# Kernel optimization log

Measured on AMD Instinct MI355X. Metric: run time of the kernel, lower is better.

## Reference

```python
import jax, jax.numpy as jnp
import numpy as np

N = 64      # num_neighbors + 1
H = 512     # hidden_size
T = 1024    # history length


def setup_inputs() -> dict:
    key = jax.random.key(0)
    ks = jax.random.split(key, 10)
    s = 1.0 / np.sqrt(H)  # PyTorch LSTM/Linear init scale
    return {
        "in_recent_values": jax.random.normal(ks[0], (N,), dtype=jnp.float32),
        "in_reputation_history": jax.random.normal(ks[1], (N, T), dtype=jnp.float32),
        # per-module LSTM params (input_size=1), gate order i,f,g,o
        "W_ih": jax.random.uniform(ks[2], (N, 4 * H), jnp.float32, -s, s),      # [N,4H] (input_size=1 squeezed)
        "W_hh": jax.random.uniform(ks[3], (N, 4 * H, H), jnp.float32, -s, s),   # [N,4H,H]
        "b_ih": jax.random.uniform(ks[4], (N, 4 * H), jnp.float32, -s, s),
        "b_hh": jax.random.uniform(ks[5], (N, 4 * H), jnp.float32, -s, s),
        # per-module output Linear(H+1 -> 1)
        "lin_W": jax.random.uniform(ks[6], (N, H + 1), jnp.float32, -s, s),
        "lin_b": jax.random.uniform(ks[7], (N,), jnp.float32, -s, s),
        # final Linear(N -> 1)
        "final_W": jax.random.uniform(ks[8], (N,), jnp.float32, -1.0 / np.sqrt(N), 1.0 / np.sqrt(N)),
        "final_b": jax.random.uniform(ks[9], (1,), jnp.float32, -1.0 / np.sqrt(N), 1.0 / np.sqrt(N)),
    }


def _batched_lstm_last_h(history, W_ih, W_hh, b_ih, b_hh):
    # history: [N,T]. Precompute input contribution for all steps: [T,N,4H]
    x_proj = history[:, :, None] * W_ih[:, None, :] + (b_ih + b_hh)[:, None, :]
    x_proj = jnp.swapaxes(x_proj, 0, 1)  # [T,N,4H]

    def step(carry, x_t):
        h, c = carry  # [N,H] each
        gates = x_t + jnp.einsum("nh,ngh->ng", h, W_hh)  # [N,4H]
        i, f, g, o = jnp.split(gates, 4, axis=-1)
        i = jax.nn.sigmoid(i)
        f = jax.nn.sigmoid(f)
        g = jnp.tanh(g)
        o = jax.nn.sigmoid(o)
        c = f * c + i * g
        h = o * jnp.tanh(c)
        return (h, c), None

    h0 = jnp.zeros((N, H), dtype=history.dtype)
    (h_last, _), _ = jax.lax.scan(step, (h0, h0), x_proj)
    return h_last  # [N,H]


def reference(in_recent_values, in_reputation_history, W_ih, W_hh, b_ih, b_hh,
              lin_W, lin_b, final_W, final_b):
    h_last = _batched_lstm_last_h(in_reputation_history, W_ih, W_hh, b_ih, b_hh)
    # per-module linear on [h_last, current_reading] -> scalar each
    feat = jnp.concatenate([h_last, in_recent_values[:, None]], axis=1)  # [N,H+1]
    per_mod = jnp.sum(feat * lin_W, axis=1) + lin_b                      # [N]
    out = per_mod @ final_W + final_b                                    # [1]
    return out
```

## Files before the change

### kernel.cpp

```cpp
#include <hip/hip_runtime.h>
#include <hip/hip_fp16.h>
#include <cstddef>

#define NMOD 64
#define HID 512
#define TSTEPS 1024
#define G4 2048

#define WOFF_PERMOD 0
#define WOFF_HX     16384
#define WOFF_W16    524288
#define W16_BYTES   ((size_t)NMOD * G4 * HID * 2)
#define WS_NEED     (WOFF_W16 + W16_BYTES)

__device__ __forceinline__ float fsig(float x)  { return 1.0f / (1.0f + __expf(-x)); }
__device__ __forceinline__ float ftanh_(float x){ return 1.0f - 2.0f / (__expf(2.0f * x) + 1.0f); }

__device__ __forceinline__ float adot2(unsigned a, unsigned b, float c) {
    float d;
    asm("v_dot2_f32_f16 %0, %1, %2, %3" : "=v"(d) : "v"(a), "v"(b), "v"(c));
    return d;
}
__device__ __forceinline__ float dot4(uint4 wv, uint4 hv, float acc) {
    acc = adot2(wv.x, hv.x, acc);
    acc = adot2(wv.y, hv.y, acc);
    acc = adot2(wv.z, hv.z, acc);
    acc = adot2(wv.w, hv.w, acc);
    return acc;
}

template<int CTRL>
__device__ __forceinline__ float dppf(float x) {
    int xi = __builtin_bit_cast(int, x);
    int r = __builtin_amdgcn_update_dpp(0, xi, CTRL, 0xF, 0xF, true);
    return __builtin_bit_cast(float, r);
}

__global__ __launch_bounds__(256) void conv_kernel(const float* __restrict__ src,
                                                   __half* __restrict__ dst) {
    const size_t i = ((size_t)blockIdx.x * 256 + threadIdx.x) * 8;
    const float4 a = *reinterpret_cast<const float4*>(src + i);
    const float4 b = *reinterpret_cast<const float4*>(src + i + 4);
    __half2 h0 = __floats2half2_rn(a.x, a.y);
    __half2 h1 = __floats2half2_rn(a.z, a.w);
    __half2 h2 = __floats2half2_rn(b.x, b.y);
    __half2 h3 = __floats2half2_rn(b.z, b.w);
    uint4 o;
    o.x = *reinterpret_cast<unsigned*>(&h0);
    o.y = *reinterpret_cast<unsigned*>(&h1);
    o.z = *reinterpret_cast<unsigned*>(&h2);
    o.w = *reinterpret_cast<unsigned*>(&h3);
    *reinterpret_cast<uint4*>(dst + i) = o;
}

__global__
__attribute__((amdgpu_flat_work_group_size(512, 512), amdgpu_waves_per_eu(2, 2)))
void lstm_res_kernel(
    const float* __restrict__ recent,
    const float* __restrict__ history,
    const float* __restrict__ W_ih,
    const float* __restrict__ b_ih,
    const float* __restrict__ b_hh,
    const float* __restrict__ lin_W,
    const float* __restrict__ lin_b,
    const unsigned* __restrict__ w16u,
    unsigned long long* hx,
    float* __restrict__ per_mod)
{
    const int bid = blockIdx.x;
    const int m = (bid & 7) * 8 + (bid >> 5);
    const int b = (bid >> 3) & 3;
    const int tid = threadIdx.x;
    const int rg = tid >> 4;
    const int cg = tid & 15;

    __shared__ unsigned w_lds[32768];
    __shared__ unsigned h_pk[256];
    __shared__ float gates_sh[512];
    __shared__ float hist_sh[TSTEPS];
    __shared__ float red_sh[8];

    for (int i = tid; i < TSTEPS; i += 512)
        hist_sh[i] = history[(size_t)m * TSTEPS + i];

    const size_t rowbase = (size_t)m * G4 * 256;
    uint4 w[12][4];
    #pragma unroll
    for (int r = 0; r < 12; ++r) {
        const int l = rg * 16 + r;
        const int gr = ((l >> 7) << 9) + (b << 7) + (l & 127);
        #pragma unroll
        for (int kk = 0; kk < 4; ++kk) {
            const int c = (((b + kk) & 3) << 4) + cg;
            w[r][kk] = *(const uint4*)(w16u + rowbase + (size_t)gr * 256 + c * 4);
        }
    }
    #pragma unroll
    for (int r2 = 0; r2 < 4; ++r2) {
        const int l = rg * 16 + 12 + r2;
        const int gr = ((l >> 7) << 9) + (b << 7) + (l & 127);
        #pragma unroll
        for (int kk = 0; kk < 4; ++kk) {
            const int c  = (((b + kk) & 3) << 4) + cg;
            const int wc = (((kk + rg) & 3) << 4) + cg;
            *(uint4*)&w_lds[((rg * 4 + r2) * 64 + wc) * 4] =
                *(const uint4*)(w16u + rowbase + (size_t)gr * 256 + c * 4);
        }
    }

    const int rev = ((cg & 1) << 3) | ((cg & 2) << 1) | ((cg & 4) >> 1) | ((cg & 8) >> 3);
    const int l_own = rg * 16 + rev;
    const int gr_own = ((l_own >> 7) << 9) + (b << 7) + (l_own & 127);
    const float wib_own  = W_ih[(size_t)m * G4 + gr_own];
    const float bias_own = b_ih[(size_t)m * G4 + gr_own] + b_hh[(size_t)m * G4 + gr_own];

    const bool is_writer = (tid < 128);
    const bool is_reader = (tid >= 128 && tid < 320);
    const int  rr    = tid - 128;
    const int  widx  = (((b + 1 + (rr >> 6)) & 3) << 6) + (rr & 63);

    float c0 = 0.0f;

    if (tid < 256) h_pk[tid] = 0u;

    gates_sh[l_own] = hist_sh[0] * wib_own + bias_own;

    for (int t = 0; t < TSTEPS - 1; ++t) {
        __syncthreads();
        const unsigned seq = (unsigned)(t + 1);
        const size_t pbase = (size_t)(seq & 1) * (NMOD * 256) + (size_t)m * 256;

        unsigned long long pv = 0;
        if (is_writer) {
            const float gi = fsig(gates_sh[tid]);
            const float gf = fsig(gates_sh[128 + tid]);
            const float gg = ftanh_(gates_sh[256 + tid]);
            const float go = fsig(gates_sh[384 + tid]);
            c0 = gf * c0 + gi * gg;
            const float hv = go * ftanh_(c0);
            const float ho = __shfl_xor(hv, 1, 64);
            if ((tid & 1) == 0) {
                __half2 hh = __floats2half2_rn(hv, ho);
                const unsigned pay = *reinterpret_cast<unsigned*>(&hh);
                const int word = tid >> 1;
                __hip_atomic_store(&hx[pbase + b * 64 + word],
                                   ((unsigned long long)seq << 32) | pay,
                                   __ATOMIC_RELAXED, __HIP_MEMORY_SCOPE_AGENT);
                h_pk[b * 64 + word] = pay;
            }
        } else if (is_reader) {
            pv = __hip_atomic_load(&hx[pbase + widx],
                                   __ATOMIC_RELAXED, __HIP_MEMORY_SCOPE_AGENT);
        }
        __syncthreads();

        float acc[16];
        #pragma unroll
        for (int r = 0; r < 16; ++r) acc[r] = 0.0f;
        {
            const uint4 hq = *(const uint4*)&h_pk[(b << 6) + cg * 4];
            #pragma unroll
            for (int r = 0; r < 12; ++r) acc[r] = dot4(w[r][0], hq, acc[r]);
            const int wc0 = ((rg & 3) << 4) + cg;
            #pragma unroll
            for (int r2 = 0; r2 < 4; ++r2) {
                const uint4 lw = *(const uint4*)&w_lds[((rg * 4 + r2) * 64 + wc0) * 4];
                acc[12 + r2] = dot4(lw, hq, acc[12 + r2]);
            }
        }

        if (is_reader) {
            while ((unsigned)(pv >> 32) != seq)
                pv = __hip_atomic_load(&hx[pbase + widx],
                                       __ATOMIC_RELAXED, __HIP_MEMORY_SCOPE_AGENT);
            h_pk[widx] = (unsigned)pv;
        }
        __syncthreads();

        #pragma unroll
        for (int kk = 1; kk < 4; ++kk) {
            const uint4 hq = *(const uint4*)&h_pk[((((b + kk) & 3)) << 6) + cg * 4];
            #pragma unroll
            for (int r = 0; r < 12; ++r) acc[r] = dot4(w[r][kk], hq, acc[r]);
            const int wc = (((kk + rg) & 3) << 4) + cg;
            #pragma unroll
            for (int r2 = 0; r2 < 4; ++r2) {
                const uint4 lw = *(const uint4*)&w_lds[((rg * 4 + r2) * 64 + wc) * 4];
                acc[12 + r2] = dot4(lw, hq, acc[12 + r2]);
            }
        }

        #pragma unroll
        for (int k = 0; k < 8; ++k) {
            const float send = (cg & 1) ? acc[k] : acc[8 + k];
            const float recv = dppf<0xB1>(send);
            acc[k] = ((cg & 1) ? acc[8 + k] : acc[k]) + recv;
        }
        #pragma unroll
        for (int k = 0; k < 4; ++k) {
            const float send = (cg & 2) ? acc[k] : acc[4 + k];
            const float recv = dppf<0x4E>(send);
            acc[k] = ((cg & 2) ? acc[4 + k] : acc[k]) + recv;
        }
        #pragma unroll
        for (int k = 0; k < 2; ++k) {
            const float send = (cg & 4) ? acc[k] : acc[2 + k];
            const float recv = __shfl_xor(send, 4, 64);
            acc[k] = ((cg & 4) ? acc[2 + k] : acc[k]) + recv;
        }
        {
            const float send = (cg & 8) ? acc[0] : acc[1];
            const float recv = __shfl_xor(send, 8, 64);
            acc[0] = ((cg & 8) ? acc[1] : acc[0]) + recv;
        }

        gates_sh[l_own] = acc[0] + hist_sh[t + 1] * wib_own + bias_own;
    }

    __syncthreads();
    {
        const unsigned seq = (unsigned)TSTEPS;
        const size_t pbase = (size_t)(seq & 1) * (NMOD * 256) + (size_t)m * 256;
        if (is_writer) {
            const float gi = fsig(gates_sh[tid]);
            const float gf = fsig(gates_sh[128 + tid]);
            const float gg = ftanh_(gates_sh[256 + tid]);
            const float go = fsig(gates_sh[384 + tid]);
            c0 = gf * c0 + gi * gg;
            const float hv = go * ftanh_(c0);
            const float ho = __shfl_xor(hv, 1, 64);
            if ((tid & 1) == 0) {
                __half2 hh = __floats2half2_rn(hv, ho);
                const unsigned pay = *reinterpret_cast<unsigned*>(&hh);
                const int word = tid >> 1;
                __hip_atomic_store(&hx[pbase + b * 64 + word],
                                   ((unsigned long long)seq << 32) | pay,
                                   __ATOMIC_RELAXED, __HIP_MEMORY_SCOPE_AGENT);
                h_pk[b * 64 + word] = pay;
            }
        }
        if (b == 0) {
            if (is_reader) {
                unsigned long long pv;
                do {
                    pv = __hip_atomic_load(&hx[pbase + widx],
                                           __ATOMIC_RELAXED, __HIP_MEMORY_SCOPE_AGENT);
                } while ((unsigned)(pv >> 32) != seq);
                h_pk[widx] = (unsigned)pv;
            }
            __syncthreads();
            float v = 0.0f;
            if (tid < 256) {
                const __half2 u = *reinterpret_cast<const __half2*>(&h_pk[tid]);
                const float* lwp = lin_W + (size_t)m * (HID + 1);
                v = __half2float(u.x) * lwp[2 * tid] + __half2float(u.y) * lwp[2 * tid + 1];
            }
            #pragma unroll
            for (int s2 = 32; s2; s2 >>= 1) v += __shfl_xor(v, s2, 64);
            if ((tid & 63) == 0) red_sh[tid >> 6] = v;
            __syncthreads();
            if (tid == 0) {
                float s = 0.0f;
                #pragma unroll
                for (int wv2 = 0; wv2 < 8; ++wv2) s += red_sh[wv2];
                s += recent[m] * lin_W[(size_t)m * (HID + 1) + HID] + lin_b[m];
                per_mod[m] = s;
            }
        }
    }
}

__global__ __launch_bounds__(1024) void lstm_module_kernel(
    const float* __restrict__ recent,
    const float* __restrict__ history,
    const float* __restrict__ W_ih,
    const float* __restrict__ W_hh,
    const float* __restrict__ b_ih,
    const float* __restrict__ b_hh,
    const float* __restrict__ lin_W,
    const float* __restrict__ lin_b,
    float* __restrict__ per_mod)
{
    const int n = blockIdx.x;
    const int tid = threadIdx.x;

    __shared__ float h_sh[HID];
    __shared__ float gates_sh[G4];
    __shared__ float wib_sh[G4];
    __shared__ float bias_sh[G4];
    __shared__ float hist_sh[TSTEPS];

    for (int i = tid; i < G4; i += 1024) {
        wib_sh[i]  = W_ih[(size_t)n * G4 + i];
        bias_sh[i] = b_ih[(size_t)n * G4 + i] + b_hh[(size_t)n * G4 + i];
    }
    for (int i = tid; i < TSTEPS; i += 1024) hist_sh[i] = history[(size_t)n * TSTEPS + i];
    if (tid < HID) h_sh[tid] = 0.0f;
    float c_reg = 0.0f;
    __syncthreads();

    const int sub = tid & 15;
    const int rid = tid >> 4;
    const float* Wbase = W_hh + (size_t)n * G4 * HID;

    for (int t = 0; t < TSTEPS; ++t) {
        const float x = hist_sh[t];
        float hreg[32];
        #pragma unroll
        for (int j = 0; j < 8; ++j) {
            const float4 hv = *reinterpret_cast<const float4*>(&h_sh[sub * 4 + j * 64]);
            hreg[4 * j + 0] = hv.x; hreg[4 * j + 1] = hv.y;
            hreg[4 * j + 2] = hv.z; hreg[4 * j + 3] = hv.w;
        }
        for (int p = 0; p < 32; ++p) {
            const int r = p * 64 + rid;
            const float* wr = Wbase + (size_t)r * HID + sub * 4;
            float acc = 0.0f;
            #pragma unroll
            for (int j = 0; j < 8; ++j) {
                const float4 wv = *reinterpret_cast<const float4*>(wr + j * 64);
                acc += wv.x * hreg[4*j+0] + wv.y * hreg[4*j+1]
                     + wv.z * hreg[4*j+2] + wv.w * hreg[4*j+3];
            }
            acc += __shfl_xor(acc, 1, 64);
            acc += __shfl_xor(acc, 2, 64);
            acc += __shfl_xor(acc, 4, 64);
            acc += __shfl_xor(acc, 8, 64);
            if (sub == 0) gates_sh[r] = acc + x * wib_sh[r] + bias_sh[r];
        }
        __syncthreads();
        if (tid < HID) {
            const float ig = fsig(gates_sh[tid]);
            const float fg = fsig(gates_sh[HID + tid]);
            const float gg = ftanh_(gates_sh[2 * HID + tid]);
            const float og = fsig(gates_sh[3 * HID + tid]);
            c_reg = fg * c_reg + ig * gg;
            h_sh[tid] = og * ftanh_(c_reg);
        }
        __syncthreads();
    }

    if (tid < HID) {
        float v = h_sh[tid] * lin_W[(size_t)n * (HID + 1) + tid];
        #pragma unroll
        for (int m2 = 32; m2; m2 >>= 1) v += __shfl_xor(v, m2, 64);
        if ((tid & 63) == 0) gates_sh[tid >> 6] = v;
    }
    __syncthreads();
    if (tid == 0) {
        float s = 0.0f;
        #pragma unroll
        for (int w = 0; w < HID / 64; ++w) s += gates_sh[w];
        s += recent[n] * lin_W[(size_t)n * (HID + 1) + HID] + lin_b[n];
        per_mod[n] = s;
    }
}

__global__ void finish_kernel(const float* __restrict__ per_mod,
                              const float* __restrict__ final_W,
                              const float* __restrict__ final_b,
                              float* __restrict__ out)
{
    const int l = threadIdx.x;
    float v = per_mod[l] * final_W[l];
    #pragma unroll
    for (int m = 32; m; m >>= 1) v += __shfl_xor(v, m, 64);
    if (l == 0) out[0] = v + final_b[0];
}

extern "C" void kernel_launch(void* const* d_in, const int* in_sizes, int n_in,
                              void* d_out, int out_size, void* d_ws, size_t ws_size,
                              hipStream_t stream) {
    const float* recent  = (const float*)d_in[0];
    const float* history = (const float*)d_in[1];
    const float* W_ih    = (const float*)d_in[2];
    const float* W_hh    = (const float*)d_in[3];
    const float* b_ih    = (const float*)d_in[4];
    const float* b_hh    = (const float*)d_in[5];
    const float* lin_W   = (const float*)d_in[6];
    const float* lin_b   = (const float*)d_in[7];
    const float* final_W = (const float*)d_in[8];
    const float* final_b = (const float*)d_in[9];
    float* out = (float*)d_out;
    float* per_mod = (float*)d_ws;

    if (ws_size >= WS_NEED) {
        __half* w16 = (__half*)((char*)d_ws + WOFF_W16);
        unsigned long long* hx = (unsigned long long*)((char*)d_ws + WOFF_HX);

        hipMemsetAsync(d_ws, 0, WOFF_W16, stream);

        const int conv_blocks = (int)((size_t)NMOD * G4 * HID / 8 / 256);
        conv_kernel<<<conv_blocks, 256, 0, stream>>>(W_hh, w16);

        lstm_res_kernel<<<NMOD * 4, 512, 0, stream>>>(
            recent, history, W_ih, b_ih, b_hh, lin_W, lin_b,
            (const unsigned*)w16, hx, per_mod);
    } else {
        lstm_module_kernel<<<NMOD, 1024, 0, stream>>>(
            recent, history, W_ih, W_hh, b_ih, b_hh, lin_W, lin_b, per_mod);
    }
    finish_kernel<<<1, 64, 0, stream>>>(per_mod, final_W, final_b, out);
}
```

Baseline: 2.444 ms.

## Replace dot2 GEMV with MFMA 16x16x32 f16 on fragment-prepacked weights

The recurrent matvec per step moves from v_dot2 instructions plus a DPP/shuffle cross-lane reduction to MFMA 16x16x32 f16 instructions. The h vector is broadcast as the B operand. The conversion kernel now writes W_hh directly in MFMA fragment order, so each wave loads its register and LDS tiles with contiguous reads. This removes the per-step butterfly reduction, but it wastes most of the MFMA columns (only one useful column) and adds MFMA latency to the serial recurrence.

Result: slower. 2.509 ms (+2.6%).

```diff
diff --git a/kernel.cpp b/kernel.cpp
--- a/kernel.cpp
+++ b/kernel.cpp
@@ -13,49 +13,52 @@
 #define W16_BYTES   ((size_t)NMOD * G4 * HID * 2)
 #define WS_NEED     (WOFF_W16 + W16_BYTES)
 
+typedef _Float16 half8_t __attribute__((ext_vector_type(8)));
+typedef float    f32x4_t __attribute__((ext_vector_type(4)));
+
 __device__ __forceinline__ float fsig(float x)  { return 1.0f / (1.0f + __expf(-x)); }
 __device__ __forceinline__ float ftanh_(float x){ return 1.0f - 2.0f / (__expf(2.0f * x) + 1.0f); }
 
-__device__ __forceinline__ float adot2(unsigned a, unsigned b, float c) {
-    float d;
-    asm("v_dot2_f32_f16 %0, %1, %2, %3" : "=v"(d) : "v"(a), "v"(b), "v"(c));
-    return d;
-}
-__device__ __forceinline__ float dot4(uint4 wv, uint4 hv, float acc) {
-    acc = adot2(wv.x, hv.x, acc);
-    acc = adot2(wv.y, hv.y, acc);
-    acc = adot2(wv.z, hv.z, acc);
-    acc = adot2(wv.w, hv.w, acc);
-    return acc;
-}
-
-template<int CTRL>
-__device__ __forceinline__ float dppf(float x) {
-    int xi = __builtin_bit_cast(int, x);
-    int r = __builtin_amdgcn_update_dpp(0, xi, CTRL, 0xF, 0xF, true);
-    return __builtin_bit_cast(float, r);
-}
-
-__global__ __launch_bounds__(256) void conv_kernel(const float* __restrict__ src,
-                                                   __half* __restrict__ dst) {
-    const size_t i = ((size_t)blockIdx.x * 256 + threadIdx.x) * 8;
-    const float4 a = *reinterpret_cast<const float4*>(src + i);
-    const float4 b = *reinterpret_cast<const float4*>(src + i + 4);
+__device__ __forceinline__ half8_t h8(uint4 u) { return __builtin_bit_cast(half8_t, u); }
+
+#define MFMA_F16(a, b, c) __builtin_amdgcn_mfma_f32_16x16x32_f16((a), (b), (c), 0, 0, 0)
+
+__global__ __launch_bounds__(256) void conv_frag_kernel(const float* __restrict__ src,
+                                                        unsigned* __restrict__ dst) {
+    const unsigned t_lin = blockIdx.x * 256 + threadIdx.x;
+    const unsigned chunk = t_lin >> 6, u = t_lin & 63;
+    const unsigned l = ((u & 3) << 4) | (u >> 2);
+    const unsigned t = (chunk << 6) | l;
+
+    const int ll = t & 63;
+    const int j  = (t >> 6) & 15;
+    const int mt = (t >> 10) & 3;
+    const int w  = (t >> 12) & 7;
+    const int b  = (t >> 15) & 3;
+    const int m  = (int)(t >> 17);
+    const int kc = (4 * b + j) & 15;
+    const int g  = ll >> 4, r16 = ll & 15;
+    const int lr = w * 64 + mt * 16 + r16;
+    const int gr = (lr >> 7) * 512 + b * 128 + (lr & 127);
+
+    const float* sp = src + ((size_t)m * G4 + gr) * HID + kc * 32 + g * 8;
+    const float4 a = *reinterpret_cast<const float4*>(sp);
+    const float4 c = *reinterpret_cast<const float4*>(sp + 4);
     __half2 h0 = __floats2half2_rn(a.x, a.y);
     __half2 h1 = __floats2half2_rn(a.z, a.w);
-    __half2 h2 = __floats2half2_rn(b.x, b.y);
-    __half2 h3 = __floats2half2_rn(b.z, b.w);
+    __half2 h2 = __floats2half2_rn(c.x, c.y);
+    __half2 h3 = __floats2half2_rn(c.z, c.w);
     uint4 o;
     o.x = *reinterpret_cast<unsigned*>(&h0);
     o.y = *reinterpret_cast<unsigned*>(&h1);
     o.z = *reinterpret_cast<unsigned*>(&h2);
     o.w = *reinterpret_cast<unsigned*>(&h3);
-    *reinterpret_cast<uint4*>(dst + i) = o;
+    *reinterpret_cast<uint4*>(dst + (size_t)t * 4) = o;
 }
 
 __global__
 __attribute__((amdgpu_flat_work_group_size(512, 512), amdgpu_waves_per_eu(2, 2)))
-void lstm_res_kernel(
+void lstm_mfma_kernel(
     const float* __restrict__ recent,
     const float* __restrict__ history,
     const float* __restrict__ W_ih,
@@ -63,7 +66,7 @@
     const float* __restrict__ b_hh,
     const float* __restrict__ lin_W,
     const float* __restrict__ lin_b,
-    const unsigned* __restrict__ w16u,
+    const unsigned* __restrict__ wf,
     unsigned long long* hx,
     float* __restrict__ per_mod)
 {
@@ -71,10 +74,12 @@
     const int m = (bid & 7) * 8 + (bid >> 5);
     const int b = (bid >> 3) & 3;
     const int tid = threadIdx.x;
-    const int rg = tid >> 4;
-    const int cg = tid & 15;
-
-    __shared__ unsigned w_lds[32768];
+    const int w   = tid >> 6;
+    const int l   = tid & 63;
+    const int g   = l >> 4;
+    const int c16 = l & 15;
+
+    __shared__ uint4 w_lds[8][4][4][64];
     __shared__ unsigned h_pk[256];
     __shared__ float gates_sh[512];
     __shared__ float hist_sh[TSTEPS];
@@ -83,47 +88,48 @@
     for (int i = tid; i < TSTEPS; i += 512)
         hist_sh[i] = history[(size_t)m * TSTEPS + i];
 
-    const size_t rowbase = (size_t)m * G4 * 256;
-    uint4 w[12][4];
+    const uint4* fb = (const uint4*)wf + (size_t)((m * 4 + b) * 8 + w) * 4096;
+    uint4 wr[4][12];
     #pragma unroll
-    for (int r = 0; r < 12; ++r) {
-        const int l = rg * 16 + r;
-        const int gr = ((l >> 7) << 9) + (b << 7) + (l & 127);
-        #pragma unroll
-        for (int kk = 0; kk < 4; ++kk) {
-            const int c = (((b + kk) & 3) << 4) + cg;
-            w[r][kk] = *(const uint4*)(w16u + rowbase + (size_t)gr * 256 + c * 4);
-        }
-    }
+    for (int mt = 0; mt < 4; ++mt)
+        #pragma unroll
+        for (int j = 0; j < 12; ++j)
+            wr[mt][j] = fb[(mt * 16 + j) * 64 + l];
     #pragma unroll
-    for (int r2 = 0; r2 < 4; ++r2) {
-        const int l = rg * 16 + 12 + r2;
-        const int gr = ((l >> 7) << 9) + (b << 7) + (l & 127);
-        #pragma unroll
-        for (int kk = 0; kk < 4; ++kk) {
-            const int c  = (((b + kk) & 3) << 4) + cg;
-            const int wc = (((kk + rg) & 3) << 4) + cg;
-            *(uint4*)&w_lds[((rg * 4 + r2) * 64 + wc) * 4] =
-                *(const uint4*)(w16u + rowbase + (size_t)gr * 256 + c * 4);
-        }
-    }
-
-    const int rev = ((cg & 1) << 3) | ((cg & 2) << 1) | ((cg & 4) >> 1) | ((cg & 8) >> 3);
-    const int l_own = rg * 16 + rev;
-    const int gr_own = ((l_own >> 7) << 9) + (b << 7) + (l_own & 127);
-    const float wib_own  = W_ih[(size_t)m * G4 + gr_own];
-    const float bias_own = b_ih[(size_t)m * G4 + gr_own] + b_hh[(size_t)m * G4 + gr_own];
+    for (int mt = 0; mt < 4; ++mt)
+        #pragma unroll
+        for (int j2 = 0; j2 < 4; ++j2)
+            w_lds[w][mt][j2][l] = fb[(mt * 16 + 12 + j2) * 64 + l];
+
+    float wib4[4], bias4[4];
+    if (c16 < 4) {
+        #pragma unroll
+        for (int e = 0; e < 4; ++e) {
+            const int lr = w * 64 + c16 * 16 + g * 4 + e;
+            const int gr = (lr >> 7) * 512 + b * 128 + (lr & 127);
+            wib4[e]  = W_ih[(size_t)m * G4 + gr];
+            bias4[e] = b_ih[(size_t)m * G4 + gr] + b_hh[(size_t)m * G4 + gr];
+        }
+    }
 
     const bool is_writer = (tid < 128);
     const bool is_reader = (tid >= 128 && tid < 320);
-    const int  rr    = tid - 128;
-    const int  widx  = (((b + 1 + (rr >> 6)) & 3) << 6) + (rr & 63);
+    const int  rr   = tid - 128;
+    const int  widx = (((b + 1 + (rr >> 6)) & 3) << 6) + (rr & 63);
 
     float c0 = 0.0f;
-
     if (tid < 256) h_pk[tid] = 0u;
-
-    gates_sh[l_own] = hist_sh[0] * wib_own + bias_own;
+    __syncthreads();
+
+    if (c16 < 4) {
+        const float x0 = hist_sh[0];
+        float4 o;
+        o.x = x0 * wib4[0] + bias4[0];
+        o.y = x0 * wib4[1] + bias4[1];
+        o.z = x0 * wib4[2] + bias4[2];
+        o.w = x0 * wib4[3] + bias4[3];
+        *reinterpret_cast<float4*>(&gates_sh[w * 64 + c16 * 16 + g * 4]) = o;
+    }
 
     for (int t = 0; t < TSTEPS - 1; ++t) {
         __syncthreads();
@@ -154,19 +160,19 @@
         }
         __syncthreads();
 
-        float acc[16];
-        #pragma unroll
-        for (int r = 0; r < 16; ++r) acc[r] = 0.0f;
-        {
-            const uint4 hq = *(const uint4*)&h_pk[(b << 6) + cg * 4];
-            #pragma unroll
-            for (int r = 0; r < 12; ++r) acc[r] = dot4(w[r][0], hq, acc[r]);
-            const int wc0 = ((rg & 3) << 4) + cg;
-            #pragma unroll
-            for (int r2 = 0; r2 < 4; ++r2) {
-                const uint4 lw = *(const uint4*)&w_lds[((rg * 4 + r2) * 64 + wc0) * 4];
-                acc[12 + r2] = dot4(lw, hq, acc[12 + r2]);
-            }
+        f32x4_t acc0 = {0.f, 0.f, 0.f, 0.f};
+        f32x4_t acc1 = {0.f, 0.f, 0.f, 0.f};
+        f32x4_t acc2 = {0.f, 0.f, 0.f, 0.f};
+        f32x4_t acc3 = {0.f, 0.f, 0.f, 0.f};
+
+        #pragma unroll
+        for (int j = 0; j < 4; ++j) {
+            const int kc = 4 * b + j;
+            const half8_t hv8 = h8(*(const uint4*)&h_pk[kc * 16 + g * 4]);
+            acc0 = MFMA_F16(h8(wr[0][j]), hv8, acc0);
+            acc1 = MFMA_F16(h8(wr[1][j]), hv8, acc1);
+            acc2 = MFMA_F16(h8(wr[2][j]), hv8, acc2);
+            acc3 = MFMA_F16(h8(wr[3][j]), hv8, acc3);
         }
 
         if (is_reader) {
@@ -178,43 +184,35 @@
         __syncthreads();
 
         #pragma unroll
-        for (int kk = 1; kk < 4; ++kk) {
-            const uint4 hq = *(const uint4*)&h_pk[((((b + kk) & 3)) << 6) + cg * 4];
-            #pragma unroll
-            for (int r = 0; r < 12; ++r) acc[r] = dot4(w[r][kk], hq, acc[r]);
-            const int wc = (((kk + rg) & 3) << 4) + cg;
-            #pragma unroll
-            for (int r2 = 0; r2 < 4; ++r2) {
-                const uint4 lw = *(const uint4*)&w_lds[((rg * 4 + r2) * 64 + wc) * 4];
-                acc[12 + r2] = dot4(lw, hq, acc[12 + r2]);
-            }
-        }
-
-        #pragma unroll
-        for (int k = 0; k < 8; ++k) {
-            const float send = (cg & 1) ? acc[k] : acc[8 + k];
-            const float recv = dppf<0xB1>(send);
-            acc[k] = ((cg & 1) ? acc[8 + k] : acc[k]) + recv;
-        }
-        #pragma unroll
-        for (int k = 0; k < 4; ++k) {
-            const float send = (cg & 2) ? acc[k] : acc[4 + k];
-            const float recv = dppf<0x4E>(send);
-            acc[k] = ((cg & 2) ? acc[4 + k] : acc[k]) + recv;
-        }
-        #pragma unroll
-        for (int k = 0; k < 2; ++k) {
-            const float send = (cg & 4) ? acc[k] : acc[2 + k];
-            const float recv = __shfl_xor(send, 4, 64);
-            acc[k] = ((cg & 4) ? acc[2 + k] : acc[k]) + recv;
-        }
-        {
-            const float send = (cg & 8) ? acc[0] : acc[1];
-            const float recv = __shfl_xor(send, 8, 64);
-            acc[0] = ((cg & 8) ? acc[1] : acc[0]) + recv;
-        }
-
-        gates_sh[l_own] = acc[0] + hist_sh[t + 1] * wib_own + bias_own;
+        for (int j = 4; j < 12; ++j) {
+            const int kc = (4 * b + j) & 15;
+            const half8_t hv8 = h8(*(const uint4*)&h_pk[kc * 16 + g * 4]);
+            acc0 = MFMA_F16(h8(wr[0][j]), hv8, acc0);
+            acc1 = MFMA_F16(h8(wr[1][j]), hv8, acc1);
+            acc2 = MFMA_F16(h8(wr[2][j]), hv8, acc2);
+            acc3 = MFMA_F16(h8(wr[3][j]), hv8, acc3);
+        }
+        #pragma unroll
+        for (int j2 = 0; j2 < 4; ++j2) {
+            const int kc = (4 * b + 12 + j2) & 15;
+            const half8_t hv8 = h8(*(const uint4*)&h_pk[kc * 16 + g * 4]);
+            acc0 = MFMA_F16(h8(w_lds[w][0][j2][l]), hv8, acc0);
+            acc1 = MFMA_F16(h8(w_lds[w][1][j2][l]), hv8, acc1);
+            acc2 = MFMA_F16(h8(w_lds[w][2][j2][l]), hv8, acc2);
+            acc3 = MFMA_F16(h8(w_lds[w][3][j2][l]), hv8, acc3);
+        }
+
+        if (c16 < 4) {
+            const f32x4_t a = (c16 == 0) ? acc0 : (c16 == 1) ? acc1
+                             : (c16 == 2) ? acc2 : acc3;
+            const float x1 = hist_sh[t + 1];
+            float4 o;
+            o.x = a[0] + x1 * wib4[0] + bias4[0];
+            o.y = a[1] + x1 * wib4[1] + bias4[1];
+            o.z = a[2] + x1 * wib4[2] + bias4[2];
+            o.w = a[3] + x1 * wib4[3] + bias4[3];
+            *reinterpret_cast<float4*>(&gates_sh[w * 64 + c16 * 16 + g * 4]) = o;
+        }
     }
 
     __syncthreads();
@@ -385,17 +383,16 @@
     float* per_mod = (float*)d_ws;
 
     if (ws_size >= WS_NEED) {
-        __half* w16 = (__half*)((char*)d_ws + WOFF_W16);
+        unsigned* wfrag = (unsigned*)((char*)d_ws + WOFF_W16);
         unsigned long long* hx = (unsigned long long*)((char*)d_ws + WOFF_HX);
 
         hipMemsetAsync(d_ws, 0, WOFF_W16, stream);
 
-        const int conv_blocks = (int)((size_t)NMOD * G4 * HID / 8 / 256);
-        conv_kernel<<<conv_blocks, 256, 0, stream>>>(W_hh, w16);
-
-        lstm_res_kernel<<<NMOD * 4, 512, 0, stream>>>(
+        conv_frag_kernel<<<32768, 256, 0, stream>>>(W_hh, wfrag);
+
+        lstm_mfma_kernel<<<NMOD * 4, 512, 0, stream>>>(
             recent, history, W_ih, b_ih, b_hh, lin_W, lin_b,
-            (const unsigned*)w16, hx, per_mod);
+            wfrag, hx, per_mod);
     } else {
         lstm_module_kernel<<<NMOD, 1024, 0, stream>>>(
             recent, history, W_ih, W_hh, b_ih, b_hh, lin_W, lin_b, per_mod);
```
